# Performance work log

Measured on AMD Instinct MI355X. Metric: run time of the kernel, lower is better.

## Reference

```python
import jax, jax.numpy as jnp
import numpy as np

NUM_HEADS = 8
NUM_LEVELS = 4
NUM_POINTS = 8
EMBED = 256
SPATIAL_SHAPES = ((92, 160), (46, 80), (23, 40), (12, 20))


def _bilinear_sample(vl, gx, gy, H, W):
    # vl: [N, d, H*W]; gx, gy: [N, Q, P], grid coords in [-1, 1]
    # matches F.grid_sample(mode='bilinear', padding_mode='zeros', align_corners=False)
    x = (gx + 1.0) * (W * 0.5) - 0.5
    y = (gy + 1.0) * (H * 0.5) - 0.5
    x0 = jnp.floor(x)
    y0 = jnp.floor(y)
    wx = x - x0
    wy = y - y0
    x0i = x0.astype(jnp.int32)
    y0i = y0.astype(jnp.int32)
    N, Q, P = gx.shape
    d = vl.shape[1]

    def gather(xi, yi):
        valid = ((xi >= 0) & (xi < W) & (yi >= 0) & (yi < H)).astype(vl.dtype)
        idx = jnp.clip(yi, 0, H - 1) * W + jnp.clip(xi, 0, W - 1)  # [N, Q, P]
        flat = jnp.broadcast_to(idx.reshape(N, 1, Q * P), (N, d, Q * P))
        got = jnp.take_along_axis(vl, flat, axis=2).reshape(N, d, Q, P)
        return got * valid[:, None]

    return (gather(x0i, y0i) * ((1 - wx) * (1 - wy))[:, None]
            + gather(x0i + 1, y0i) * (wx * (1 - wy))[:, None]
            + gather(x0i, y0i + 1) * ((1 - wx) * wy)[:, None]
            + gather(x0i + 1, y0i + 1) * (wx * wy)[:, None])


def _forward(query, value, reference_points, spatial_shapes,
             W_off, b_off, W_attn, b_attn, W_val, b_val, W_out, b_out):
    shapes = np.asarray(spatial_shapes)  # static per-level (H, W)
    bs, Q, C = query.shape
    H, Lv, P = NUM_HEADS, NUM_LEVELS, NUM_POINTS
    d = C // H
    # value projection, split into heads: [bs*H, d, Ltot]
    v = value @ W_val + b_val
    v = v.reshape(bs, -1, H, d).transpose(0, 2, 3, 1).reshape(bs * H, d, -1)
    # sampling offsets [bs, Q, H, Lv, P, 2]
    off = (query @ W_off + b_off).reshape(bs, Q, H, Lv, P, 2)
    # attention weights, softmax over Lv*P
    aw = jax.nn.softmax((query @ W_attn + b_attn).reshape(bs, Q, H, Lv * P), axis=-1)
    aw = aw.reshape(bs, Q, H, Lv, P).transpose(0, 2, 1, 3, 4).reshape(bs * H, Q, Lv, P)
    # normalize offsets by level (W, H)
    norm = jnp.asarray([[w_, h_] for h_, w_ in shapes], dtype=query.dtype)  # [Lv, 2]
    loc = reference_points[:, :, None, :, None, :] + off / norm[None, None, None, :, None, :]
    grids = (2.0 * loc - 1.0).transpose(0, 2, 1, 3, 4, 5).reshape(bs * H, Q, Lv, P, 2)
    out = jnp.zeros((bs * H, d, Q), dtype=query.dtype)
    start = 0
    for lvl in range(Lv):
        H_l, W_l = int(shapes[lvl, 0]), int(shapes[lvl, 1])
        vl = v[:, :, start:start + H_l * W_l]
        g = grids[:, :, lvl]  # [bs*H, Q, P, 2]
        s = _bilinear_sample(vl, g[..., 0], g[..., 1], H_l, W_l)  # [bs*H, d, Q, P]
        out = out + jnp.einsum('ndqp,nqp->ndq', s, aw[:, :, lvl])
        start += H_l * W_l
    out = out.reshape(bs, H, d, Q).transpose(0, 3, 1, 2).reshape(bs, Q, C)
    return out @ W_out + b_out


def setup_inputs() -> dict:
    key = jax.random.key(0)
    ks = jax.random.split(key, 9)
    bs, Q = 6, 4096  # 6 cameras x (64x64 BEV queries)
    Ltot = sum(h * w for h, w in SPATIAL_SHAPES)  # 19560
    HLP2 = NUM_HEADS * NUM_LEVELS * NUM_POINTS * 2  # 512
    HLP = NUM_HEADS * NUM_LEVELS * NUM_POINTS  # 256
    s = 0.02
    return {
        "query": jax.random.normal(ks[0], (bs, Q, EMBED), jnp.float32),
        "value": jax.random.normal(ks[1], (bs, Ltot, EMBED), jnp.float32),
        "reference_points": jax.random.uniform(ks[2], (bs, Q, NUM_LEVELS, 2), jnp.float32),
        "spatial_shapes": jnp.asarray(SPATIAL_SHAPES, jnp.int32),
        "W_off": s * jax.random.normal(ks[3], (EMBED, HLP2), jnp.float32),
        "b_off": s * jax.random.normal(ks[4], (HLP2,), jnp.float32),
        "W_attn": s * jax.random.normal(ks[5], (EMBED, HLP), jnp.float32),
        "b_attn": s * jax.random.normal(ks[6], (HLP,), jnp.float32),
        "W_val": s * jax.random.normal(ks[7], (EMBED, EMBED), jnp.float32),
        "b_val": jnp.zeros((EMBED,), jnp.float32),
        "W_out": s * jax.random.normal(ks[8], (EMBED, EMBED), jnp.float32),
        "b_out": jnp.zeros((EMBED,), jnp.float32),
    }


def reference(query, value, reference_points, spatial_shapes,
              W_off, b_off, W_attn, b_attn, W_val, b_val, W_out, b_out):
    return _forward(query, value, reference_points, spatial_shapes,
                    W_off, b_off, W_attn, b_attn, W_val, b_val, W_out, b_out)
```

## Files before the change

### kernel.cpp

```cpp
#include <hip/hip_runtime.h>
#include <hip/hip_fp16.h>
#include <stdint.h>

#define BS 6
#define NQ 4096
#define NH 8
#define EMB 256
#define LTOT 19560
#define ROWS_V 117360
#define ROWS_VP 117376
#define ROWS_Q 24576

typedef __attribute__((ext_vector_type(8))) short bf16x8;
typedef __attribute__((ext_vector_type(4))) float floatx4;
typedef __attribute__((ext_vector_type(8))) unsigned short ushort8v;

__device__ __forceinline__ ushort f2bf(float f) {
    union { float f; uint32_t i; } c; c.f = f;
    uint32_t r = c.i + 0x7FFFu + ((c.i >> 16) & 1u);
    return (ushort)(r >> 16);
}
__device__ __forceinline__ ushort f2h(float f) {
    __half h = __float2half(f);
    union { __half h; ushort u; } c; c.h = h; return c.u;
}

__device__ __forceinline__ void gll16(const ushort* g, ushort* l) {
    __builtin_amdgcn_global_load_lds(
        (const __attribute__((address_space(1))) void*)g,
        (__attribute__((address_space(3))) void*)l, 16, 0, 0);
}

template<int L>
__device__ __forceinline__ float bcastf(float x) {
    return __int_as_float(
        __builtin_amdgcn_ds_swizzle(__float_as_int(x), 0x1C | (L << 5)));
}
template<int L>
__device__ __forceinline__ uint32_t bcastu(uint32_t x) {
    return (uint32_t)__builtin_amdgcn_ds_swizzle((int)x, 0x1C | (L << 5));
}

__device__ __forceinline__ void fmx_lo(float& acc, float w, uint32_t u) {
    asm("v_fma_mix_f32 %0, %1, %2, %0 op_sel:[0,0,0] op_sel_hi:[0,1,0]"
        : "+v"(acc) : "v"(w), "v"(u));
}
__device__ __forceinline__ void fmx_hi(float& acc, float w, uint32_t u) {
    asm("v_fma_mix_f32 %0, %1, %2, %0 op_sel:[0,1,0] op_sel_hi:[0,1,0]"
        : "+v"(acc) : "v"(w), "v"(u));
}

__global__ __launch_bounds__(256) void cast_bf16(
    const float* __restrict__ in, ushort* __restrict__ out, int n)
{
    int i = (blockIdx.x * 256 + threadIdx.x) * 8;
    if (i >= n) return;
    float4 f0 = *(const float4*)(in + i);
    float4 f1 = *(const float4*)(in + i + 4);
    ushort8v r;
    r[0] = f2bf(f0.x); r[1] = f2bf(f0.y); r[2] = f2bf(f0.z); r[3] = f2bf(f0.w);
    r[4] = f2bf(f1.x); r[5] = f2bf(f1.y); r[6] = f2bf(f1.z); r[7] = f2bf(f1.w);
    *(ushort8v*)(out + i) = r;
}

__global__ __launch_bounds__(256) void cast_t(
    const float* __restrict__ W, ushort* __restrict__ Wt, int N_)
{
    int id = blockIdx.x * 256 + threadIdx.x;
    if (id >= 256 * N_) return;
    int n = id >> 8;
    int k = id & 255;
    Wt[id] = f2bf(W[(size_t)k * N_ + n]);
}

__global__ __launch_bounds__(768) void bias_concat(
    const float* __restrict__ b_off, const float* __restrict__ b_attn,
    float* __restrict__ bcat)
{
    int i = threadIdx.x;
    bcat[i] = (i < 512) ? b_off[i] : b_attn[i - 512];
}

__global__ __launch_bounds__(512) void vgemm(
    const float* __restrict__ A,
    const ushort* __restrict__ Bt,
    const float* __restrict__ bias,
    ushort* __restrict__ C)
{
    constexpr int K = 256, N = 256, M = ROWS_V;
    __shared__ ushort As[128 * 32];
    __shared__ ushort Bs[256 * 32];

    const int t = threadIdx.x;
    const int w = t >> 6;
    const int lane = t & 63;
    const int bm = blockIdx.x * 128;
    const int wm = (w >> 2) * 64;
    const int wn = (w & 3) * 64;

    const int arow = t >> 2;
    const int acol = (t & 3) * 8;
    const bool rowok = (bm + arow) < M;
    const float* Ap = A + (size_t)(bm + arow) * K + acol;
    ushort* Asw = &As[arow * 32 + acol];

    const int srow = lane >> 2;
    const int scol = (lane & 3) * 8;
    const ushort* Bg0 = Bt + (size_t)(w * 32 + srow) * K + scol;
    const ushort* Bg1 = Bt + (size_t)(w * 32 + 16 + srow) * K + scol;
    ushort* Bl0 = &Bs[(w * 32) * 32];
    ushort* Bl1 = &Bs[(w * 32 + 16) * 32];

    const ushort* apt = &As[(wm + (lane & 15)) * 32 + (lane >> 4) * 8];
    const ushort* bpt = &Bs[(wn + (lane & 15)) * 32 + (lane >> 4) * 8];

    floatx4 acc[4][4] = {};

    for (int kt = 0; kt < K; kt += 32) {
        float4 f0, f1;
        if (rowok) {
            f0 = *(const float4*)(Ap + kt);
            f1 = *(const float4*)(Ap + kt + 4);
        } else {
            f0 = make_float4(0.f, 0.f, 0.f, 0.f);
            f1 = f0;
        }
        __syncthreads();
        gll16(Bg0 + kt, Bl0);
        gll16(Bg1 + kt, Bl1);
        ushort8v u;
        u[0] = f2bf(f0.x); u[1] = f2bf(f0.y); u[2] = f2bf(f0.z); u[3] = f2bf(f0.w);
        u[4] = f2bf(f1.x); u[5] = f2bf(f1.y); u[6] = f2bf(f1.z); u[7] = f2bf(f1.w);
        *(ushort8v*)Asw = u;
        __syncthreads();

        bf16x8 a[4], b[4];
        #pragma unroll
        for (int i = 0; i < 4; ++i) {
            a[i] = *(const bf16x8*)(apt + i * 16 * 32);
            b[i] = *(const bf16x8*)(bpt + i * 16 * 32);
        }
        #pragma unroll
        for (int i = 0; i < 4; ++i)
            #pragma unroll
            for (int j = 0; j < 4; ++j)
                acc[i][j] = __builtin_amdgcn_mfma_f32_16x16x32_bf16(
                    a[i], b[j], acc[i][j], 0, 0, 0);
    }

    const int crow = (lane >> 4) * 4;
    const int ccol = lane & 15;
    #pragma unroll
    for (int j = 0; j < 4; ++j) {
        int gcol = wn + j * 16 + ccol;
        float bv = bias[gcol];
        #pragma unroll
        for (int i = 0; i < 4; ++i) {
            #pragma unroll
            for (int r = 0; r < 4; ++r) {
                int grow = bm + wm + i * 16 + crow + r;
                if (grow < M)
                    C[(size_t)grow * N + gcol] = f2h(acc[i][j][r] + bv);
            }
        }
    }
}

__global__ __launch_bounds__(256) void gemm_bt(
    const ushort* __restrict__ A,
    const ushort* __restrict__ Bt,
    const float* __restrict__ bias,
    float* __restrict__ C, int M, int N)
{
    constexpr int K = 256;
    __shared__ ushort As[128 * 32];
    __shared__ ushort Bs[128 * 32];

    const int t = threadIdx.x;
    const int w = t >> 6;
    const int lane = t & 63;
    const int bm = blockIdx.x * 128;
    const int bn = blockIdx.y * 128;
    const int wm = (w >> 1) * 64;
    const int wn = (w & 1) * 64;

    floatx4 acc[4][4] = {};

    const int srow = lane >> 2;
    const int scol = (lane & 3) * 8;
    const ushort* Ag0 = A + (size_t)(bm + (w * 2 + 0) * 16 + srow) * K + scol;
    const ushort* Ag1 = A + (size_t)(bm + (w * 2 + 1) * 16 + srow) * K + scol;
    const ushort* Bg0 = Bt + (size_t)(bn + (w * 2 + 0) * 16 + srow) * K + scol;
    const ushort* Bg1 = Bt + (size_t)(bn + (w * 2 + 1) * 16 + srow) * K + scol;
    ushort* Al0 = &As[(w * 2 + 0) * 512];
    ushort* Al1 = &As[(w * 2 + 1) * 512];
    ushort* Bl0 = &Bs[(w * 2 + 0) * 512];
    ushort* Bl1 = &Bs[(w * 2 + 1) * 512];

    const ushort* apt = &As[(wm + (lane & 15)) * 32 + (lane >> 4) * 8];
    const ushort* bpt = &Bs[(wn + (lane & 15)) * 32 + (lane >> 4) * 8];

    for (int kt = 0; kt < K; kt += 32) {
        __syncthreads();
        gll16(Ag0 + kt, Al0);
        gll16(Ag1 + kt, Al1);
        gll16(Bg0 + kt, Bl0);
        gll16(Bg1 + kt, Bl1);
        __syncthreads();

        bf16x8 a[4], b[4];
        #pragma unroll
        for (int i = 0; i < 4; ++i) {
            a[i] = *(const bf16x8*)(apt + i * 16 * 32);
            b[i] = *(const bf16x8*)(bpt + i * 16 * 32);
        }
        #pragma unroll
        for (int i = 0; i < 4; ++i)
            #pragma unroll
            for (int j = 0; j < 4; ++j)
                acc[i][j] = __builtin_amdgcn_mfma_f32_16x16x32_bf16(
                    a[i], b[j], acc[i][j], 0, 0, 0);
    }

    const int crow = (lane >> 4) * 4;
    const int ccol = lane & 15;
    #pragma unroll
    for (int j = 0; j < 4; ++j) {
        int gcol = bn + wn + j * 16 + ccol;
        float bv = bias[gcol];
        #pragma unroll
        for (int i = 0; i < 4; ++i) {
            #pragma unroll
            for (int r = 0; r < 4; ++r) {
                int grow = bm + wm + i * 16 + crow + r;
                if (grow < M)
                    C[(size_t)grow * N + gcol] = acc[i][j][r] + bv;
            }
        }
    }
}

__global__ __launch_bounds__(256) void sampler4(
    const ushort* __restrict__ v,
    const float* __restrict__ qp,
    const float* __restrict__ ref,
    ushort* __restrict__ agg)
{
    __shared__ char ballast[49152];
    if (blockIdx.x > 0x7FFFFFF0u) {
        ballast[threadIdx.x] = (char)threadIdx.x;
        agg[0] = (ushort)ballast[(threadIdx.x * 37) & 4095];
    }

    const int tid = threadIdx.x;
    const int g = blockIdx.x * 64 + (tid >> 2);
    const int st = tid & 3;
    const int h = g & 7;
    const int bq = g >> 3;
    const int b = blockIdx.x >> 9;

    const int Wl = 160 >> st;
    const int Hl = (st == 3) ? 12 : (92 >> st);
    const int Sl = (st == 0) ? 0 : (st == 1) ? 14720 : (st == 2) ? 18400 : 19320;

    float px[8], py[8];
    {
        const float* offp = qp + (size_t)bq * 768 + h * 64 + st * 16;
        float o[16];
        #pragma unroll
        for (int i = 0; i < 4; ++i)
            *(float4*)&o[i * 4] = *(const float4*)(offp + i * 4);
        float2 rf = *(const float2*)(ref + (size_t)bq * 8 + st * 2);
        const float fW = (float)Wl, fH = (float)Hl;
        #pragma unroll
        for (int i = 0; i < 8; ++i) {
            px[i] = fmaf(rf.x, fW, o[2 * i]) - 0.5f;
            py[i] = fmaf(rf.y, fH, o[2 * i + 1]) - 0.5f;
        }
    }

    float a8[8];
    {
        const float* lp = qp + (size_t)bq * 768 + 512 + h * 32 + st * 8;
        *(float4*)&a8[0] = *(const float4*)(lp);
        *(float4*)&a8[4] = *(const float4*)(lp + 4);
        float m = a8[0];
        #pragma unroll
        for (int i = 1; i < 8; ++i) m = fmaxf(m, a8[i]);
        m = fmaxf(m, __shfl_xor(m, 1, 4));
        m = fmaxf(m, __shfl_xor(m, 2, 4));
        float s = 0.f;
        #pragma unroll
        for (int i = 0; i < 8; ++i) { a8[i] = __expf(a8[i] - m); s += a8[i]; }
        s += __shfl_xor(s, 1, 4);
        s += __shfl_xor(s, 2, 4);
        float inv = 1.f / s;
        #pragma unroll
        for (int i = 0; i < 8; ++i) a8[i] *= inv;
    }

    const char* vb = (const char*)(v + (size_t)b * (LTOT * EMB));
    const uint32_t coffB = (uint32_t)(h * 64 + st * 16);

    float acc[8] = {0.f, 0.f, 0.f, 0.f, 0.f, 0.f, 0.f, 0.f};

    #pragma unroll
    for (int idx = 0; idx < 8; ++idx) {
        float px_ = px[idx], py_ = py[idx];
        float x0f = floorf(px_), y0f = floorf(py_);
        float wx = px_ - x0f, wy = py_ - y0f;
        int x0 = (int)x0f, y0 = (int)y0f;
        int x1 = x0 + 1, y1 = y0 + 1;
        float vx0 = ((uint32_t)x0 < (uint32_t)Wl) ? 1.f : 0.f;
        float vx1 = ((uint32_t)x1 < (uint32_t)Wl) ? 1.f : 0.f;
        float vy0 = ((uint32_t)y0 < (uint32_t)Hl) ? 1.f : 0.f;
        float vy1 = ((uint32_t)y1 < (uint32_t)Hl) ? 1.f : 0.f;
        int cx0 = min(max(x0, 0), Wl - 1);
        int cx1 = min(max(x1, 0), Wl - 1);
        int cy0 = min(max(y0, 0), Hl - 1);
        int cy1 = min(max(y1, 0), Hl - 1);
        float aw = a8[idx];
        float omx = 1.f - wx, omy = 1.f - wy;
        float omya = omy * aw, wya = wy * aw;
        float w00 = omx * omya * (vx0 * vy0);
        float w10 = wx  * omya * (vx1 * vy0);
        float w01 = omx * wya  * (vx0 * vy1);
        float w11 = wx  * wya  * (vx1 * vy1);
        int r0 = Sl + cy0 * Wl;
        int r1 = Sl + cy1 * Wl;
        uint32_t e00 = (uint32_t)(r0 + cx0) << 9;
        uint32_t e10 = (uint32_t)(r0 + cx1) << 9;
        uint32_t e01 = (uint32_t)(r1 + cx0) << 9;
        uint32_t e11 = (uint32_t)(r1 + cx1) << 9;

        #define ACCMIX(w_, c_) \
            fmx_lo(acc[0], w_, c_.x); fmx_hi(acc[1], w_, c_.x); \
            fmx_lo(acc[2], w_, c_.y); fmx_hi(acc[3], w_, c_.y); \
            fmx_lo(acc[4], w_, c_.z); fmx_hi(acc[5], w_, c_.z); \
            fmx_lo(acc[6], w_, c_.w); fmx_hi(acc[7], w_, c_.w);
        #define DO_LEVEL(L) { \
            float W00 = bcastf<L>(w00), W10 = bcastf<L>(w10); \
            float W01 = bcastf<L>(w01), W11 = bcastf<L>(w11); \
            uint32_t E00 = bcastu<L>(e00), E10 = bcastu<L>(e10); \
            uint32_t E01 = bcastu<L>(e01), E11 = bcastu<L>(e11); \
            uint4 c00 = *(const uint4*)(vb + (E00 + coffB)); \
            uint4 c10 = *(const uint4*)(vb + (E10 + coffB)); \
            uint4 c01 = *(const uint4*)(vb + (E01 + coffB)); \
            uint4 c11 = *(const uint4*)(vb + (E11 + coffB)); \
            ACCMIX(W00, c00); ACCMIX(W10, c10); \
            ACCMIX(W01, c01); ACCMIX(W11, c11); }
        DO_LEVEL(0)
        DO_LEVEL(1)
        DO_LEVEL(2)
        DO_LEVEL(3)
        #undef DO_LEVEL
        #undef ACCMIX
    }

    ushort8v r;
    #pragma unroll
    for (int i = 0; i < 8; ++i) r[i] = f2bf(acc[i]);
    *(ushort8v*)(agg + (size_t)bq * 256 + h * 32 + st * 8) = r;
}

extern "C" void kernel_launch(void* const* d_in, const int* in_sizes, int n_in,
                              void* d_out, int out_size, void* d_ws, size_t ws_size,
                              hipStream_t stream) {
    const float* query  = (const float*)d_in[0];
    const float* value  = (const float*)d_in[1];
    const float* refpts = (const float*)d_in[2];
    const float* W_off  = (const float*)d_in[4];
    const float* b_off  = (const float*)d_in[5];
    const float* W_attn = (const float*)d_in[6];
    const float* b_attn = (const float*)d_in[7];
    const float* W_val  = (const float*)d_in[8];
    const float* b_val  = (const float*)d_in[9];
    const float* W_out  = (const float*)d_in[10];
    const float* b_out  = (const float*)d_in[11];
    float* out = (float*)d_out;

    char* ws = (char*)d_ws;
    ushort* v_bf   = (ushort*)(ws);
    ushort* q_bf   = (ushort*)(ws + 60096512ull);
    float*  qp     = (float*) (ws + 72679424ull);
    ushort* agg_bf = (ushort*)(ws + 148176896ull);
    ushort* Wvt    = (ushort*)(ws + 160759808ull);
    ushort* Wq     = (ushort*)(ws + 160890880ull);
    ushort* Wot    = (ushort*)(ws + 161284096ull);
    float*  bcat   = (float*) (ws + 161415168ull);

    cast_t<<<(256 * 256) / 256, 256, 0, stream>>>(W_val, Wvt, 256);
    cast_t<<<(256 * 512) / 256, 256, 0, stream>>>(W_off, Wq, 512);
    cast_t<<<(256 * 256) / 256, 256, 0, stream>>>(W_attn, Wq + 512 * 256, 256);
    cast_t<<<(256 * 256) / 256, 256, 0, stream>>>(W_out, Wot, 256);
    bias_concat<<<1, 768, 0, stream>>>(b_off, b_attn, bcat);
    cast_bf16<<<(ROWS_Q * EMB / 8) / 256, 256, 0, stream>>>(
        query, q_bf, ROWS_Q * EMB);

    vgemm<<<ROWS_VP / 128, 512, 0, stream>>>(value, Wvt, b_val, v_bf);

    gemm_bt<<<dim3(ROWS_Q / 128, 6), 256, 0, stream>>>(
        q_bf, Wq, bcat, qp, ROWS_Q, 768);

    sampler4<<<(ROWS_Q * NH) / 64, 256, 0, stream>>>(
        v_bf, qp, refpts, agg_bf);

    gemm_bt<<<dim3(ROWS_Q / 128, 2), 256, 0, stream>>>(
        agg_bf, Wot, b_out, out, ROWS_Q, 256);
}
```

Measured before the change: 446.7 us.

## Fuse weight prep kernels, cast query in-GEMM, store projections as fp16

```diff
diff --git a/kernel.cpp b/kernel.cpp
--- a/kernel.cpp
+++ b/kernel.cpp
@@ -24,6 +24,9 @@
     __half h = __float2half(f);
     union { __half h; ushort u; } c; c.h = h; return c.u;
 }
+__device__ __forceinline__ float h2f(ushort u) {
+    union { ushort u; __half h; } c; c.u = u; return __half2float(c.h);
+}
 
 __device__ __forceinline__ void gll16(const ushort* g, ushort* l) {
     __builtin_amdgcn_global_load_lds(
@@ -50,35 +53,39 @@
         : "+v"(acc) : "v"(w), "v"(u));
 }
 
-__global__ __launch_bounds__(256) void cast_bf16(
-    const float* __restrict__ in, ushort* __restrict__ out, int n)
-{
-    int i = (blockIdx.x * 256 + threadIdx.x) * 8;
-    if (i >= n) return;
-    float4 f0 = *(const float4*)(in + i);
-    float4 f1 = *(const float4*)(in + i + 4);
-    ushort8v r;
-    r[0] = f2bf(f0.x); r[1] = f2bf(f0.y); r[2] = f2bf(f0.z); r[3] = f2bf(f0.w);
-    r[4] = f2bf(f1.x); r[5] = f2bf(f1.y); r[6] = f2bf(f1.z); r[7] = f2bf(f1.w);
-    *(ushort8v*)(out + i) = r;
-}
-
-__global__ __launch_bounds__(256) void cast_t(
-    const float* __restrict__ W, ushort* __restrict__ Wt, int N_)
+__global__ __launch_bounds__(256) void prep(
+    const float* __restrict__ W_val, const float* __restrict__ W_off,
+    const float* __restrict__ W_attn, const float* __restrict__ W_out,
+    const float* __restrict__ b_off, const float* __restrict__ b_attn,
+    ushort* __restrict__ Wvt, ushort* __restrict__ Wq,
+    ushort* __restrict__ Wot, float* __restrict__ bcat)
 {
     int id = blockIdx.x * 256 + threadIdx.x;
-    if (id >= 256 * N_) return;
-    int n = id >> 8;
-    int k = id & 255;
-    Wt[id] = f2bf(W[(size_t)k * N_ + n]);
-}
-
-__global__ __launch_bounds__(768) void bias_concat(
-    const float* __restrict__ b_off, const float* __restrict__ b_attn,
-    float* __restrict__ bcat)
-{
-    int i = threadIdx.x;
-    bcat[i] = (i < 512) ? b_off[i] : b_attn[i - 512];
+    if (id < 65536) {
+        int n = id >> 8, k = id & 255;
+        Wvt[id] = f2bf(W_val[k * 256 + n]);
+        return;
+    }
+    id -= 65536;
+    if (id < 131072) {
+        int n = id >> 8, k = id & 255;
+        Wq[id] = f2bf(W_off[k * 512 + n]);
+        return;
+    }
+    id -= 131072;
+    if (id < 65536) {
+        int n = id >> 8, k = id & 255;
+        Wq[131072 + id] = f2bf(W_attn[k * 256 + n]);
+        return;
+    }
+    id -= 65536;
+    if (id < 65536) {
+        int n = id >> 8, k = id & 255;
+        Wot[id] = f2bf(W_out[k * 256 + n]);
+        return;
+    }
+    id -= 65536;
+    if (id < 768) bcat[id] = (id < 512) ? b_off[id] : b_attn[id - 512];
 }
 
 __global__ __launch_bounds__(512) void vgemm(
@@ -162,6 +169,88 @@
                 if (grow < M)
                     C[(size_t)grow * N + gcol] = f2h(acc[i][j][r] + bv);
             }
+        }
+    }
+}
+
+__global__ __launch_bounds__(256) void qgemm(
+    const float* __restrict__ A,
+    const ushort* __restrict__ Bt,
+    const float* __restrict__ bias,
+    ushort* __restrict__ C)
+{
+    constexpr int K = 256, N = 768;
+    __shared__ ushort As[128 * 32];
+    __shared__ ushort Bs[128 * 32];
+
+    const int t = threadIdx.x;
+    const int w = t >> 6;
+    const int lane = t & 63;
+    const int bm = blockIdx.x * 128;
+    const int bn = blockIdx.y * 128;
+    const int wm = (w >> 1) * 64;
+    const int wn = (w & 1) * 64;
+
+    const int arow = t >> 1;
+    const int acol = (t & 1) * 16;
+    const float* Ap = A + (size_t)(bm + arow) * K + acol;
+    ushort* Asw = &As[arow * 32 + acol];
+
+    const int srow = lane >> 2;
+    const int scol = (lane & 3) * 8;
+    const ushort* Bg0 = Bt + (size_t)(bn + w * 32 + srow) * K + scol;
+    const ushort* Bg1 = Bt + (size_t)(bn + w * 32 + 16 + srow) * K + scol;
+    ushort* Bl0 = &Bs[(w * 32) * 32];
+    ushort* Bl1 = &Bs[(w * 32 + 16) * 32];
+
+    const ushort* apt = &As[(wm + (lane & 15)) * 32 + (lane >> 4) * 8];
+    const ushort* bpt = &Bs[(wn + (lane & 15)) * 32 + (lane >> 4) * 8];
+
+    floatx4 acc[4][4] = {};
+
+    for (int kt = 0; kt < K; kt += 32) {
+        float4 f0 = *(const float4*)(Ap + kt);
+        float4 f1 = *(const float4*)(Ap + kt + 4);
+        float4 f2 = *(const float4*)(Ap + kt + 8);
+        float4 f3 = *(const float4*)(Ap + kt + 12);
+        __syncthreads();
+        gll16(Bg0 + kt, Bl0);
+        gll16(Bg1 + kt, Bl1);
+        ushort8v u0, u1;
+        u0[0] = f2bf(f0.x); u0[1] = f2bf(f0.y); u0[2] = f2bf(f0.z); u0[3] = f2bf(f0.w);
+        u0[4] = f2bf(f1.x); u0[5] = f2bf(f1.y); u0[6] = f2bf(f1.z); u0[7] = f2bf(f1.w);
+        u1[0] = f2bf(f2.x); u1[1] = f2bf(f2.y); u1[2] = f2bf(f2.z); u1[3] = f2bf(f2.w);
+        u1[4] = f2bf(f3.x); u1[5] = f2bf(f3.y); u1[6] = f2bf(f3.z); u1[7] = f2bf(f3.w);
+        *(ushort8v*)Asw = u0;
+        *(ushort8v*)(Asw + 8) = u1;
+        __syncthreads();
+
+        bf16x8 a[4], b[4];
+        #pragma unroll
+        for (int i = 0; i < 4; ++i) {
+            a[i] = *(const bf16x8*)(apt + i * 16 * 32);
+            b[i] = *(const bf16x8*)(bpt + i * 16 * 32);
+        }
+        #pragma unroll
+        for (int i = 0; i < 4; ++i)
+            #pragma unroll
+            for (int j = 0; j < 4; ++j)
+                acc[i][j] = __builtin_amdgcn_mfma_f32_16x16x32_bf16(
+                    a[i], b[j], acc[i][j], 0, 0, 0);
+    }
+
+    const int crow = (lane >> 4) * 4;
+    const int ccol = lane & 15;
+    #pragma unroll
+    for (int j = 0; j < 4; ++j) {
+        int gcol = bn + wn + j * 16 + ccol;
+        float bv = bias[gcol];
+        #pragma unroll
+        for (int i = 0; i < 4; ++i) {
+            int grow = bm + wm + i * 16 + crow;
+            #pragma unroll
+            for (int r = 0; r < 4; ++r)
+                C[(size_t)(grow + r) * N + gcol] = f2h(acc[i][j][r] + bv);
         }
     }
 }
@@ -242,7 +331,7 @@
 
 __global__ __launch_bounds__(256) void sampler4(
     const ushort* __restrict__ v,
-    const float* __restrict__ qp,
+    const ushort* __restrict__ qp,
     const float* __restrict__ ref,
     ushort* __restrict__ agg)
 {
@@ -263,27 +352,28 @@
     const int Hl = (st == 3) ? 12 : (92 >> st);
     const int Sl = (st == 0) ? 0 : (st == 1) ? 14720 : (st == 2) ? 18400 : 19320;
 
+    const ushort* qrow = qp + (size_t)bq * 768;
+
     float px[8], py[8];
     {
-        const float* offp = qp + (size_t)bq * 768 + h * 64 + st * 16;
-        float o[16];
-        #pragma unroll
-        for (int i = 0; i < 4; ++i)
-            *(float4*)&o[i * 4] = *(const float4*)(offp + i * 4);
+        ushort8v uo0 = *(const ushort8v*)(qrow + h * 64 + st * 16);
+        ushort8v uo1 = *(const ushort8v*)(qrow + h * 64 + st * 16 + 8);
         float2 rf = *(const float2*)(ref + (size_t)bq * 8 + st * 2);
         const float fW = (float)Wl, fH = (float)Hl;
         #pragma unroll
-        for (int i = 0; i < 8; ++i) {
-            px[i] = fmaf(rf.x, fW, o[2 * i]) - 0.5f;
-            py[i] = fmaf(rf.y, fH, o[2 * i + 1]) - 0.5f;
+        for (int i = 0; i < 4; ++i) {
+            px[i]     = fmaf(rf.x, fW, h2f(uo0[2 * i]))     - 0.5f;
+            py[i]     = fmaf(rf.y, fH, h2f(uo0[2 * i + 1])) - 0.5f;
+            px[i + 4] = fmaf(rf.x, fW, h2f(uo1[2 * i]))     - 0.5f;
+            py[i + 4] = fmaf(rf.y, fH, h2f(uo1[2 * i + 1])) - 0.5f;
         }
     }
 
     float a8[8];
     {
-        const float* lp = qp + (size_t)bq * 768 + 512 + h * 32 + st * 8;
-        *(float4*)&a8[0] = *(const float4*)(lp);
-        *(float4*)&a8[4] = *(const float4*)(lp + 4);
+        ushort8v ul = *(const ushort8v*)(qrow + 512 + h * 32 + st * 8);
+        #pragma unroll
+        for (int i = 0; i < 8; ++i) a8[i] = h2f(ul[i]);
         float m = a8[0];
         #pragma unroll
         for (int i = 1; i < 8; ++i) m = fmaxf(m, a8[i]);
@@ -381,26 +471,19 @@
 
     char* ws = (char*)d_ws;
     ushort* v_bf   = (ushort*)(ws);
-    ushort* q_bf   = (ushort*)(ws + 60096512ull);
-    float*  qp     = (float*) (ws + 72679424ull);
+    ushort* qp     = (ushort*)(ws + 72679424ull);
     ushort* agg_bf = (ushort*)(ws + 148176896ull);
     ushort* Wvt    = (ushort*)(ws + 160759808ull);
     ushort* Wq     = (ushort*)(ws + 160890880ull);
     ushort* Wot    = (ushort*)(ws + 161284096ull);
     float*  bcat   = (float*) (ws + 161415168ull);
 
-    cast_t<<<(256 * 256) / 256, 256, 0, stream>>>(W_val, Wvt, 256);
-    cast_t<<<(256 * 512) / 256, 256, 0, stream>>>(W_off, Wq, 512);
-    cast_t<<<(256 * 256) / 256, 256, 0, stream>>>(W_attn, Wq + 512 * 256, 256);
-    cast_t<<<(256 * 256) / 256, 256, 0, stream>>>(W_out, Wot, 256);
-    bias_concat<<<1, 768, 0, stream>>>(b_off, b_attn, bcat);
-    cast_bf16<<<(ROWS_Q * EMB / 8) / 256, 256, 0, stream>>>(
-        query, q_bf, ROWS_Q * EMB);
+    prep<<<1283, 256, 0, stream>>>(W_val, W_off, W_attn, W_out,
+                                   b_off, b_attn, Wvt, Wq, Wot, bcat);
 
     vgemm<<<ROWS_VP / 128, 512, 0, stream>>>(value, Wvt, b_val, v_bf);
 
-    gemm_bt<<<dim3(ROWS_Q / 128, 6), 256, 0, stream>>>(
-        q_bf, Wq, bcat, qp, ROWS_Q, 768);
+    qgemm<<<dim3(ROWS_Q / 128, 6), 256, 0, stream>>>(query, Wq, bcat, qp);
 
     sampler4<<<(ROWS_Q * NH) / 64, 256, 0, stream>>>(
         v_bf, qp, refpts, agg_bf);
```

Result: faster. 423.2 us (-5.3%).
